# Kernel optimization log

Measured on AMD Instinct MI355X. Metric: run time of the kernel, lower is better.

Reference implementation:

```python
import jax, jax.numpy as jnp
from jax import lax
import numpy as np

T, N, E = 8, 20000, 640000
D_IN, H, K = 2, 64, 3


def setup_inputs() -> dict:
    key = jax.random.key(0)
    ks = jax.random.split(key, 10)
    x = jax.random.normal(ks[0], (T, N, D_IN), dtype=jnp.float32)
    edge_idx = jax.random.randint(ks[1], (T, 2, E), 0, N, dtype=jnp.int64)
    edge_attr = jax.random.uniform(ks[2], (T, E), dtype=jnp.float32)
    Fin = D_IN + H
    s = 0.05
    Wr = jax.random.normal(ks[3], (K, Fin, H), dtype=jnp.float32) * s
    Wu = jax.random.normal(ks[4], (K, Fin, H), dtype=jnp.float32) * s
    Wc = jax.random.normal(ks[5], (K, Fin, H), dtype=jnp.float32) * s
    br = jnp.zeros((H,), dtype=jnp.float32)
    bu = jnp.zeros((H,), dtype=jnp.float32)
    bc = jnp.zeros((H,), dtype=jnp.float32)
    return {"x": x, "edge_idx": edge_idx, "edge_attr": edge_attr,
            "Wr": Wr, "br": br, "Wu": Wu, "bu": bu, "Wc": Wc, "bc": bc}


def reference(x, edge_idx, edge_attr, Wr, br, Wu, bu, Wc, bc):
    n = x.shape[1]
    k_hops = Wr.shape[0]

    def cheb(v, src, dst, wn, W, b):
        # Chebyshev recursion on scaled Laplacian (PyG ChebConv, lambda_max=2)
        def prop(t):
            return jax.ops.segment_sum(wn[:, None] * t[src], dst, num_segments=n)
        Tx0 = v
        out = Tx0 @ W[0]
        Tx1 = prop(Tx0)
        out = out + Tx1 @ W[1]
        for kk in range(2, k_hops):
            Tx2 = 2.0 * prop(Tx1) - Tx0
            out = out + Tx2 @ W[kk]
            Tx0, Tx1 = Tx1, Tx2
        return out + b

    def step(h, inp):
        x_t, ei, w_t = inp
        src, dst = ei[0], ei[1]
        # sym-normalized Laplacian, scaled by 2/lambda_max=1; self-loop weight is 0
        deg = jax.ops.segment_sum(w_t, src, num_segments=n)
        safe = jnp.where(deg > 0, deg, 1.0)
        dinv = jnp.where(deg > 0, lax.rsqrt(safe), 0.0)
        wn = -dinv[src] * w_t * dinv[dst]
        comb = jnp.concatenate([x_t, h], axis=1)
        r = jax.nn.sigmoid(cheb(comb, src, dst, wn, Wr, br))
        u = jax.nn.sigmoid(cheb(comb, src, dst, wn, Wu, bu))
        c = jnp.tanh(cheb(jnp.concatenate([x_t, r * h], axis=1), src, dst, wn, Wc, bc))
        h_new = u * h + (1.0 - u) * c
        return h_new, None

    h0 = jnp.zeros((n, br.shape[0]), dtype=x.dtype)
    h_final, _ = lax.scan(step, h0, (x, edge_idx, edge_attr))
    return h_final
```

## Files before the change

### kernel.cpp

```cpp
#include <hip/hip_runtime.h>

#define NN 20000
#define EE 640000
#define TT 8
#define HF 64
#define AS 232
#define PBLK 5000
#define TILE 2560
#define NBIN 250
#define BWID 80
#define ECAP 3072
#define LCAP 24
#define DCH 32

typedef _Float16 f16;
typedef unsigned int uint;
typedef __attribute__((ext_vector_type(8))) _Float16 half8;
typedef __attribute__((ext_vector_type(4))) float floatx4;

__device__ __forceinline__ float lo16f(uint v) { return (float)__builtin_bit_cast(f16, (unsigned short)(v & 0xffff)); }
__device__ __forceinline__ float hi16f(uint v) { return (float)__builtin_bit_cast(f16, (unsigned short)(v >> 16)); }
__device__ __forceinline__ uint pk16(float a, float b) {
    unsigned short ua = __builtin_bit_cast(unsigned short, (f16)a);
    unsigned short ub = __builtin_bit_cast(unsigned short, (f16)b);
    return (uint)ua | ((uint)ub << 16);
}

__global__ __launch_bounds__(256) void k_prepW(
    const float* __restrict__ Wr, const float* __restrict__ Wu, const float* __restrict__ Wc,
    f16* __restrict__ Wp)
{
    int idx = blockIdx.x * 256 + threadIdx.x;
    if (idx >= 12 * 7 * 64) return;
    int lane = idx & 63;
    int kb = (idx >> 6) % 7;
    int nb = (idx >> 6) / 7;
    int col = nb * 16 + (lane & 15);
    int g = col >> 6, jj = col & 63;
    const float* W = (g == 0) ? Wr : (g == 1 ? Wu : Wc);
    half8 v;
    #pragma unroll
    for (int e = 0; e < 8; e++) {
        int k = kb * 32 + ((lane >> 4) << 3) + e;
        float val = 0.f;
        if (k < 192)      { int hop = k >> 6; int i = 2 + (k & 63); val = W[(hop * 66 + i) * 64 + jj]; }
        else if (k < 198) { int q = k - 192;  int hop = q >> 1;     val = W[(hop * 66 + (q & 1)) * 64 + jj]; }
        v[e] = (f16)val;
    }
    *(half8*)&Wp[(size_t)idx * 8] = v;
}

__global__ __launch_bounds__(256) void k_deg(
    const int* __restrict__ eidx, const float* __restrict__ eatt, int t0,
    float* __restrict__ deg)
{
    __shared__ float dl[NN];
    int tl = blockIdx.x >> 5, chunk = blockIdx.x & (DCH - 1);
    int tid = threadIdx.x;
    for (int n = tid; n < NN; n += 256) dl[n] = 0.f;
    __syncthreads();
    const int*   src = eidx + (size_t)(t0 + tl) * 2 * EE + chunk * (EE / DCH);
    const float* w   = eatt + (size_t)(t0 + tl) * EE + chunk * (EE / DCH);
    for (int e = tid; e < EE / DCH; e += 256) {
        int s = __builtin_nontemporal_load(&src[e]);
        float wv = __builtin_nontemporal_load(&w[e]);
        atomicAdd(&dl[s], wv);
    }
    __syncthreads();
    float* dg = deg + (size_t)tl * NN;
    for (int n = tid; n < NN; n += 256) {
        float v = dl[n];
        if (v != 0.f) atomicAdd(&dg[n], v);
    }
}

__global__ __launch_bounds__(256) void k_dinv_setx(
    float* __restrict__ deg, float* __restrict__ dinv,
    const float* __restrict__ x4, uint* __restrict__ xf4, int* __restrict__ binptr)
{
    int idx = blockIdx.x * 256 + threadIdx.x;
    if (idx < 4 * NBIN) binptr[idx] = 0;
    if (idx >= 4 * NN) return;
    float d = deg[idx];
    deg[idx] = 0.f;
    dinv[idx] = d > 0.f ? 1.f / sqrtf(d) : 0.f;
    int tl = idx / NN, n = idx - tl * NN;
    xf4[idx] = pk16(x4[(size_t)tl * NN * 2 + 2 * n], x4[(size_t)tl * NN * 2 + 2 * n + 1]);
}

__global__ __launch_bounds__(256) void k_bin(
    const int* __restrict__ eidx, const float* __restrict__ eatt, int t0,
    int* __restrict__ binptr, uint2* __restrict__ ebuf)
{
    __shared__ uint2 buf[NBIN][LCAP];
    __shared__ int lcnt[NBIN];
    __shared__ int scan[256];
    __shared__ int gb[NBIN];
    int tid = threadIdx.x;
    if (tid < NBIN) lcnt[tid] = 0;
    __syncthreads();
    int tl = blockIdx.x / 250, tile = blockIdx.x % 250;
    const int*   src = eidx + (size_t)(t0 + tl) * 2 * EE + tile * TILE;
    const int*   dst = src + EE;
    const float* w   = eatt + (size_t)(t0 + tl) * EE + tile * TILE;
    int* bp = binptr + tl * NBIN;
    size_t ebase = (size_t)tl * NBIN * ECAP;
    #pragma unroll
    for (int i = 0; i < TILE / 256; i++) {
        int e = i * 256 + tid;
        int s = __builtin_nontemporal_load(&src[e]);
        int d = __builtin_nontemporal_load(&dst[e]);
        float wv = __builtin_nontemporal_load(&w[e]);
        int bin = d / BWID;
        uint2 ent = make_uint2(((uint)d << 16) | (uint)s, __float_as_uint(wv));
        int p = atomicAdd(&lcnt[bin], 1);
        if (p < LCAP) buf[bin][p] = ent;
        else {
            int gp = atomicAdd(&bp[bin], 1);
            if (gp < ECAP) ebuf[ebase + (size_t)bin * ECAP + gp] = ent;
        }
    }
    __syncthreads();
    int c = (tid < NBIN) ? (lcnt[tid] < LCAP ? lcnt[tid] : LCAP) : 0;
    scan[tid] = c;
    __syncthreads();
    #pragma unroll
    for (int o = 1; o < 256; o <<= 1) {
        int v = (tid >= o) ? scan[tid - o] : 0;
        __syncthreads();
        scan[tid] += v;
        __syncthreads();
    }
    if (c > 0) gb[tid] = atomicAdd(&bp[tid], c);
    __syncthreads();
    int total = scan[255];
    for (int i = tid; i < total; i += 256) {
        int lo = 0, hi = 255;
        #pragma unroll
        for (int it = 0; it < 8; it++) { int mid = (lo + hi) >> 1; if (scan[mid] > i) hi = mid; else lo = mid + 1; }
        int p = i - (lo ? scan[lo - 1] : 0);
        int gp = gb[lo] + p;
        if (gp < ECAP) ebuf[ebase + (size_t)lo * ECAP + gp] = buf[lo][p];
    }
}

__global__ __launch_bounds__(256) void k_csr(
    const uint2* __restrict__ ebuf, const int* __restrict__ binptr,
    const float* __restrict__ dinv,
    uint* __restrict__ entries, int* __restrict__ row_ptr, int* __restrict__ cnt)
{
    __shared__ uint proc[ECAP];
    __shared__ unsigned char lnb[ECAP];
    __shared__ uint staged[ECAP];
    __shared__ int lcnt[BWID], loff[BWID];
    int tl = blockIdx.x / NBIN, b = blockIdx.x % NBIN, tid = threadIdx.x;
    int nume = binptr[tl * NBIN + b]; if (nume > ECAP) nume = ECAP;
    const float* dv = dinv + (size_t)tl * NN;
    size_t base = (size_t)(tl * NBIN + b) * ECAP;
    if (tid < BWID) lcnt[tid] = 0;
    __syncthreads();
    for (int i = tid; i < nume; i += 256) {
        uint2 ent = ebuf[base + i];
        int s = ent.x & 0xffff;
        int d = ent.x >> 16;
        float wv = __uint_as_float(ent.y);
        float wn = -dv[s] * wv * dv[d];
        unsigned short wb = __builtin_bit_cast(unsigned short, (f16)wn);
        proc[i] = ((uint)wb << 16) | (uint)s;
        int ln = d - b * BWID;
        lnb[i] = (unsigned char)ln;
        atomicAdd(&lcnt[ln], 1);
    }
    __syncthreads();
    if (tid == 0) {
        int run = 0;
        for (int i = 0; i < BWID; i++) { loff[i] = run; run += lcnt[i]; }
    }
    __syncthreads();
    if (tid < BWID) {
        int n = tl * NN + b * BWID + tid;
        row_ptr[n] = (int)base + loff[tid];
        cnt[n] = lcnt[tid];
    }
    __syncthreads();
    for (int i = tid; i < nume; i += 256) {
        int p = atomicAdd(&loff[lnb[i]], 1);
        staged[p] = proc[i];
    }
    __syncthreads();
    for (int i = tid; i < nume; i += 256)
        entries[base + i] = staged[i];
}

__global__ __launch_bounds__(256) void k_prop(
    const f16* __restrict__ src_mat, const f16* __restrict__ base,
    f16* __restrict__ dst,
    const int* __restrict__ row_ptr, const int* __restrict__ cnt,
    const uint* __restrict__ entries,
    float alpha, float beta,
    const uint* __restrict__ xsrc, const uint* __restrict__ xbase,
    uint* __restrict__ xdst)
{
    __shared__ uint wnbuf[4][128];
    int ws = threadIdx.x >> 6, lane = threadIdx.x & 63;
    int node = blockIdx.x * 4 + ws;
    int m = cnt[node]; if (m > 128) m = 128;
    int st = row_ptr[node];
    int mp = (m + 15) & ~15;
    for (int idx = lane; idx < mp; idx += 64)
        wnbuf[ws][idx] = (idx < m) ? entries[st + idx] : 0u;
    asm volatile("s_waitcnt lgkmcnt(0)" ::: "memory");

    int j = lane & 31, q = lane >> 5;
    float acc0[8], acc1[8];
    #pragma unroll
    for (int k = 0; k < 8; k++) { acc0[k] = 0.f; acc1[k] = 0.f; }
    for (int e = 0; e < mp; e += 16) {
        uint ee[8], rr[8];
        #pragma unroll
        for (int k = 0; k < 8; k++) ee[k] = wnbuf[ws][e + 2 * k + q];
        #pragma unroll
        for (int k = 0; k < 8; k++) rr[k] = *(const uint*)&src_mat[(size_t)(ee[k] & 0xffff) * HF + 2 * j];
        #pragma unroll
        for (int k = 0; k < 8; k++) {
            float w = hi16f(ee[k]);
            acc0[k] += w * lo16f(rr[k]);
            acc1[k] += w * hi16f(rr[k]);
        }
    }
    float s0 = ((acc0[0] + acc0[1]) + (acc0[2] + acc0[3])) + ((acc0[4] + acc0[5]) + (acc0[6] + acc0[7]));
    float s1 = ((acc1[0] + acc1[1]) + (acc1[2] + acc1[3])) + ((acc1[4] + acc1[5]) + (acc1[6] + acc1[7]));
    s0 += __shfl_xor(s0, 32);
    s1 += __shfl_xor(s1, 32);
    if (q == 0) {
        float r0 = alpha * s0, r1 = alpha * s1;
        if (base) {
            uint bv = *(const uint*)&base[(size_t)node * HF + 2 * j];
            r0 += beta * lo16f(bv);
            r1 += beta * hi16f(bv);
        }
        *(uint*)&dst[(size_t)node * HF + 2 * j] = pk16(r0, r1);
    }

    if (xdst) {
        float xa0 = 0.f, xa1 = 0.f;
        for (int i = lane; i < mp; i += 64) {
            uint ent = wnbuf[ws][i];
            uint xv = xsrc[ent & 0xffff];
            float wn = hi16f(ent);
            xa0 += wn * lo16f(xv);
            xa1 += wn * hi16f(xv);
        }
        #pragma unroll
        for (int o = 32; o >= 1; o >>= 1) {
            xa0 += __shfl_xor(xa0, o);
            xa1 += __shfl_xor(xa1, o);
        }
        if (lane == 0) {
            float r0 = alpha * xa0, r1 = alpha * xa1;
            if (xbase) { uint bv = xbase[node]; r0 += beta * lo16f(bv); r1 += beta * hi16f(bv); }
            xdst[node] = pk16(r0, r1);
        }
    }
}

__device__ __forceinline__ void stage_A(
    f16 (*At)[AS], int n0, int tid, int nthr,
    const f16* h0, const f16* h1, const f16* h2,
    const uint* x0, const uint* x1, const uint* x2)
{
    for (int idx = tid; idx < 64 * 8 * 3; idx += nthr) {
        int a = idx >> 9, r = (idx >> 3) & 63, s = idx & 7;
        const f16* src = (a == 0) ? h0 : (a == 1 ? h1 : h2);
        int gn = n0 + r;
        half8 v = {0, 0, 0, 0, 0, 0, 0, 0};
        if (gn < NN) v = *(const half8*)&src[(size_t)gn * HF + s * 8];
        *(half8*)&At[r][a * 64 + s * 8] = v;
    }
    for (int idx = tid; idx < 64 * 17; idx += nthr) {
        int r = idx / 17, c = idx % 17;
        *(uint*)((char*)&At[r][198] + 4 * c) = 0u;
    }
    for (int idx = tid; idx < 64 * 3; idx += nthr) {
        int r = idx & 63, a = idx >> 6;
        const uint* src = (a == 0) ? x0 : (a == 1 ? x1 : x2);
        int gn = n0 + r;
        uint v = 0;
        if (gn < NN) v = src[gn];
        *(uint*)&At[r][192 + 2 * a] = v;
    }
}

#define MFMA16(a, b, c) __builtin_amdgcn_mfma_f32_16x16x32_f16(a, b, c, 0, 0, 0)

__global__ __launch_bounds__(512) void k_ru(
    const f16* __restrict__ hA, const f16* __restrict__ t1, const f16* __restrict__ t2,
    const uint* __restrict__ xf, const uint* __restrict__ t1x, const uint* __restrict__ t2x,
    const f16* __restrict__ Wp, const float* __restrict__ br, const float* __restrict__ bu,
    f16* __restrict__ u_out, f16* __restrict__ rh_out)
{
    __shared__ __attribute__((aligned(16))) f16 At[64][AS];
    int n0 = blockIdx.x * 64;
    int tid = threadIdx.x;
    stage_A(At, n0, tid, 512, hA, t1, t2, xf, t1x, t2x);
    __syncthreads();

    int wid = tid >> 6, lane = tid & 63;
    int mrow = (wid & 1) * 32;
    int nb0 = (wid >> 1) * 2;
    int arow = mrow + (lane & 15);
    int koff = (lane >> 4) << 3;
    floatx4 z = {0.f, 0.f, 0.f, 0.f};
    floatx4 acc00 = z, acc01 = z, acc10 = z, acc11 = z;
    #pragma unroll
    for (int kb = 0; kb < 7; kb++) {
        half8 a0 = *(const half8*)&At[arow][kb * 32 + koff];
        half8 a1 = *(const half8*)&At[arow + 16][kb * 32 + koff];
        half8 b0 = *(const half8*)&Wp[(size_t)(((nb0    ) * 7 + kb) * 64 + lane) * 8];
        half8 b1 = *(const half8*)&Wp[(size_t)(((nb0 + 1) * 7 + kb) * 64 + lane) * 8];
        acc00 = MFMA16(a0, b0, acc00);
        acc10 = MFMA16(a1, b0, acc10);
        acc01 = MFMA16(a0, b1, acc01);
        acc11 = MFMA16(a1, b1, acc11);
    }
    bool isR = nb0 < 4;
    #pragma unroll
    for (int mi = 0; mi < 2; mi++) {
        #pragma unroll
        for (int ni = 0; ni < 2; ni++) {
            floatx4 a = (mi == 0) ? (ni == 0 ? acc00 : acc01) : (ni == 0 ? acc10 : acc11);
            int jj = ((nb0 + ni) * 16 + (lane & 15)) & 63;
            float bias = isR ? br[jj] : bu[jj];
            int nodeb = n0 + mrow + mi * 16 + ((lane >> 4) << 2);
            #pragma unroll
            for (int e = 0; e < 4; e++) {
                int node = nodeb + e;
                if (node < NN) {
                    float s = 1.f / (1.f + __expf(-(a[e] + bias)));
                    if (isR) {
                        float hv = (float)hA[(size_t)node * HF + jj];
                        rh_out[(size_t)node * HF + jj] = (f16)(s * hv);
                    } else {
                        u_out[(size_t)node * HF + jj] = (f16)s;
                    }
                }
            }
        }
    }
}

__global__ __launch_bounds__(256) void k_c(
    const f16* __restrict__ rh, const f16* __restrict__ t1c, const f16* __restrict__ t2c,
    const uint* __restrict__ xf, const uint* __restrict__ t1x, const uint* __restrict__ t2x,
    const f16* __restrict__ Wp, const float* __restrict__ bc,
    const f16* __restrict__ u_in, const float* __restrict__ h_in,
    float* __restrict__ h_out, f16* __restrict__ hA_out)
{
    __shared__ __attribute__((aligned(16))) f16 At[64][AS];
    int n0 = blockIdx.x * 64;
    int tid = threadIdx.x;
    stage_A(At, n0, tid, 256, rh, t1c, t2c, xf, t1x, t2x);
    __syncthreads();

    int wid = tid >> 6, lane = tid & 63;
    int mrow = (wid & 1) * 32;
    int nb0 = 8 + ((wid >> 1) << 1);
    int arow = mrow + (lane & 15);
    int koff = (lane >> 4) << 3;
    floatx4 z = {0.f, 0.f, 0.f, 0.f};
    floatx4 acc00 = z, acc01 = z, acc10 = z, acc11 = z;
    #pragma unroll
    for (int kb = 0; kb < 7; kb++) {
        half8 a0 = *(const half8*)&At[arow][kb * 32 + koff];
        half8 a1 = *(const half8*)&At[arow + 16][kb * 32 + koff];
        half8 b0 = *(const half8*)&Wp[(size_t)(((nb0    ) * 7 + kb) * 64 + lane) * 8];
        half8 b1 = *(const half8*)&Wp[(size_t)(((nb0 + 1) * 7 + kb) * 64 + lane) * 8];
        acc00 = MFMA16(a0, b0, acc00);
        acc10 = MFMA16(a1, b0, acc10);
        acc01 = MFMA16(a0, b1, acc01);
        acc11 = MFMA16(a1, b1, acc11);
    }
    #pragma unroll
    for (int mi = 0; mi < 2; mi++) {
        #pragma unroll
        for (int ni = 0; ni < 2; ni++) {
            floatx4 a = (mi == 0) ? (ni == 0 ? acc00 : acc01) : (ni == 0 ? acc10 : acc11);
            int jj = (nb0 + ni) * 16 + (lane & 15) - 128;
            float bias = bc[jj];
            int nodeb = n0 + mrow + mi * 16 + ((lane >> 4) << 2);
            #pragma unroll
            for (int e = 0; e < 4; e++) {
                int node = nodeb + e;
                if (node < NN) {
                    float c = tanhf(a[e] + bias);
                    float uu = (float)u_in[(size_t)node * HF + jj];
                    float hp = h_in[(size_t)node * HF + jj];
                    float hn = uu * hp + (1.f - uu) * c;
                    h_out[(size_t)node * HF + jj] = hn;
                    hA_out[(size_t)node * HF + jj] = (f16)hn;
                }
            }
        }
    }
}


extern "C" void kernel_launch(void* const* d_in, const int* in_sizes, int n_in,
                              void* d_out, int out_size, void* d_ws, size_t ws_size,
                              hipStream_t stream)
{
    const float* x    = (const float*)d_in[0];
    const int*   eidx = (const int*)d_in[1];
    const float* eatt = (const float*)d_in[2];
    const float* Wr   = (const float*)d_in[3];
    const float* br   = (const float*)d_in[4];
    const float* Wu   = (const float*)d_in[5];
    const float* bu   = (const float*)d_in[6];
    const float* Wc   = (const float*)d_in[7];
    const float* bc   = (const float*)d_in[8];

    char* ws = (char*)d_ws;
    size_t off = 0;
    auto alloc = [&](size_t bytes) -> void* {
        void* p = ws + off;
        off += (bytes + 255) & ~(size_t)255;
        return p;
    };
    const size_t FB = (size_t)NN * HF * 2;
    float* h_f32  = (float*)alloc((size_t)NN * HF * 4);
    f16*   hA     = (f16*)alloc(FB);
    f16*   t1     = (f16*)alloc(FB);
    f16*   t2     = (f16*)alloc(FB);
    f16*   rh     = (f16*)alloc(FB);
    f16*   u      = (f16*)alloc(FB);
    float* deg    = (float*)alloc((size_t)4 * NN * 4);
    float* dinv   = (float*)alloc((size_t)4 * NN * 4);
    uint*  xf     = (uint*)alloc((size_t)TT * NN * 4);
    uint*  t1x    = (uint*)alloc((size_t)NN * 4);
    uint*  t2x    = (uint*)alloc((size_t)NN * 4);
    int*   binptr = (int*)alloc((size_t)4 * NBIN * 4);
    uint2* ebuf   = (uint2*)alloc((size_t)4 * NBIN * ECAP * 8);
    uint*  entr   = (uint*)alloc((size_t)4 * NBIN * ECAP * 4);
    int*   rowp   = (int*)alloc((size_t)4 * NN * 4);
    int*   cnt    = (int*)alloc((size_t)4 * NN * 4);
    f16*   Wp     = (f16*)alloc((size_t)12 * 7 * 64 * 8 * 2);

    hipMemsetAsync(h_f32, 0, (size_t)NN * HF * 4 + FB, stream);
    hipMemsetAsync(deg, 0, (size_t)4 * NN * 4, stream);
    k_prepW<<<21, 256, 0, stream>>>(Wr, Wu, Wc, Wp);

    const int GB = (NN + 63) / 64;
    const int DB = (4 * NN + 255) / 256;

    for (int half = 0; half < 2; ++half) {
        int t0 = half * 4;
        k_deg      <<<4 * DCH, 256, 0, stream>>>(eidx, eatt, t0, deg);
        k_dinv_setx<<<DB, 256, 0, stream>>>(deg, dinv,
                                            x + (size_t)t0 * NN * 2, xf + (size_t)t0 * NN, binptr);
        k_bin      <<<1000, 256, 0, stream>>>(eidx, eatt, t0, binptr, ebuf);
        k_csr      <<<1000, 256, 0, stream>>>(ebuf, binptr, dinv, entr, rowp, cnt);

        for (int tl = 0; tl < 4; ++tl) {
            int t = t0 + tl;
            const int* rp = rowp + (size_t)tl * NN;
            const int* cp = cnt + (size_t)tl * NN;
            uint* xft = xf + (size_t)t * NN;

            k_prop<<<PBLK, 256, 0, stream>>>(hA, nullptr, t1, rp, cp, entr, 1.f,  0.f, xft, nullptr, t1x);
            k_prop<<<PBLK, 256, 0, stream>>>(t1, hA,      t2, rp, cp, entr, 2.f, -1.f, t1x, xft,     t2x);

            k_ru<<<GB, 512, 0, stream>>>(hA, t1, t2, xft, t1x, t2x, Wp, br, bu, u, rh);

            k_prop<<<PBLK, 256, 0, stream>>>(rh, nullptr, t1, rp, cp, entr, 1.f,  0.f, nullptr, nullptr, nullptr);
            k_prop<<<PBLK, 256, 0, stream>>>(t1, rh,      t2, rp, cp, entr, 2.f, -1.f, nullptr, nullptr, nullptr);

            float* hdst = (t == TT - 1) ? (float*)d_out : h_f32;
            k_c<<<GB, 256, 0, stream>>>(rh, t1, t2, xft, t1x, t2x, Wp, bc, u, h_f32, hdst, hA);
        }
    }
}
```

Before: 811.1 us.

## Reorder candidate Chebyshev conv as transform-then-propagate via Clenshaw, fuse GRU update

```diff
diff --git a/kernel.cpp b/kernel.cpp
--- a/kernel.cpp
+++ b/kernel.cpp
@@ -5,13 +5,15 @@
 #define TT 8
 #define HF 64
 #define AS 232
+#define ACS 104
+#define BSS 194
 #define PBLK 5000
 #define TILE 2560
 #define NBIN 250
 #define BWID 80
 #define ECAP 3072
 #define LCAP 24
-#define DCH 32
+#define DCH 128
 
 typedef _Float16 f16;
 typedef unsigned int uint;
@@ -28,26 +30,48 @@
 
 __global__ __launch_bounds__(256) void k_prepW(
     const float* __restrict__ Wr, const float* __restrict__ Wu, const float* __restrict__ Wc,
-    f16* __restrict__ Wp)
+    f16* __restrict__ Wp, f16* __restrict__ Wcp)
 {
     int idx = blockIdx.x * 256 + threadIdx.x;
-    if (idx >= 12 * 7 * 64) return;
-    int lane = idx & 63;
-    int kb = (idx >> 6) % 7;
-    int nb = (idx >> 6) / 7;
-    int col = nb * 16 + (lane & 15);
-    int g = col >> 6, jj = col & 63;
-    const float* W = (g == 0) ? Wr : (g == 1 ? Wu : Wc);
+    if (idx < 8 * 7 * 64) {
+        int lane = idx & 63;
+        int kb = (idx >> 6) % 7;
+        int nb = (idx >> 6) / 7;
+        int col = nb * 16 + (lane & 15);
+        int g = col >> 6, jj = col & 63;
+        const float* W = (g == 0) ? Wr : Wu;
+        half8 v;
+        #pragma unroll
+        for (int e = 0; e < 8; e++) {
+            int k = kb * 32 + ((lane >> 4) << 3) + e;
+            float val = 0.f;
+            if (k < 192)      { int hop = k >> 6; int i = 2 + (k & 63); val = W[(hop * 66 + i) * 64 + jj]; }
+            else if (k < 198) { int q = k - 192;  int hop = q >> 1;     val = W[(hop * 66 + (q & 1)) * 64 + jj]; }
+            v[e] = (f16)val;
+        }
+        *(half8*)&Wp[(size_t)idx * 8] = v;
+        return;
+    }
+    int idx2 = idx - 8 * 7 * 64;
+    if (idx2 >= 12 * 3 * 64) return;
+    int lane = idx2 & 63;
+    int kb = (idx2 >> 6) % 3;
+    int nbc = (idx2 >> 6) / 3;
+    int col = nbc * 16 + (lane & 15);
+    int mode = col >> 6, j = col & 63;
     half8 v;
     #pragma unroll
     for (int e = 0; e < 8; e++) {
         int k = kb * 32 + ((lane >> 4) << 3) + e;
         float val = 0.f;
-        if (k < 192)      { int hop = k >> 6; int i = 2 + (k & 63); val = W[(hop * 66 + i) * 64 + jj]; }
-        else if (k < 198) { int q = k - 192;  int hop = q >> 1;     val = W[(hop * 66 + (q & 1)) * 64 + jj]; }
+        if (k < 66) {
+            if (mode == 0)      val = Wc[(0 * 66 + k) * 64 + j] - Wc[(2 * 66 + k) * 64 + j];
+            else if (mode == 1) val = Wc[(1 * 66 + k) * 64 + j];
+            else                val = Wc[(2 * 66 + k) * 64 + j];
+        }
         v[e] = (f16)val;
     }
-    *(half8*)&Wp[(size_t)idx * 8] = v;
+    *(half8*)&Wcp[(size_t)idx2 * 8] = v;
 }
 
 __global__ __launch_bounds__(256) void k_deg(
@@ -55,7 +79,7 @@
     float* __restrict__ deg)
 {
     __shared__ float dl[NN];
-    int tl = blockIdx.x >> 5, chunk = blockIdx.x & (DCH - 1);
+    int tl = blockIdx.x >> 7, chunk = blockIdx.x & (DCH - 1);
     int tid = threadIdx.x;
     for (int n = tid; n < NN; n += 256) dl[n] = 0.f;
     __syncthreads();
@@ -192,6 +216,32 @@
         entries[base + i] = staged[i];
 }
 
+__device__ __forceinline__ void gather64(
+    const f16* __restrict__ src_mat, const uint* wnb, int mp, int j, int q,
+    float& s0, float& s1)
+{
+    float acc0[8], acc1[8];
+    #pragma unroll
+    for (int k = 0; k < 8; k++) { acc0[k] = 0.f; acc1[k] = 0.f; }
+    for (int e = 0; e < mp; e += 16) {
+        uint ee[8], rr[8];
+        #pragma unroll
+        for (int k = 0; k < 8; k++) ee[k] = wnb[e + 2 * k + q];
+        #pragma unroll
+        for (int k = 0; k < 8; k++) rr[k] = *(const uint*)&src_mat[(size_t)(ee[k] & 0xffff) * HF + 2 * j];
+        #pragma unroll
+        for (int k = 0; k < 8; k++) {
+            float w = hi16f(ee[k]);
+            acc0[k] += w * lo16f(rr[k]);
+            acc1[k] += w * hi16f(rr[k]);
+        }
+    }
+    s0 = ((acc0[0] + acc0[1]) + (acc0[2] + acc0[3])) + ((acc0[4] + acc0[5]) + (acc0[6] + acc0[7]));
+    s1 = ((acc1[0] + acc1[1]) + (acc1[2] + acc1[3])) + ((acc1[4] + acc1[5]) + (acc1[6] + acc1[7]));
+    s0 += __shfl_xor(s0, 32);
+    s1 += __shfl_xor(s1, 32);
+}
+
 __global__ __launch_bounds__(256) void k_prop(
     const f16* __restrict__ src_mat, const f16* __restrict__ base,
     f16* __restrict__ dst,
@@ -212,26 +262,8 @@
     asm volatile("s_waitcnt lgkmcnt(0)" ::: "memory");
 
     int j = lane & 31, q = lane >> 5;
-    float acc0[8], acc1[8];
-    #pragma unroll
-    for (int k = 0; k < 8; k++) { acc0[k] = 0.f; acc1[k] = 0.f; }
-    for (int e = 0; e < mp; e += 16) {
-        uint ee[8], rr[8];
-        #pragma unroll
-        for (int k = 0; k < 8; k++) ee[k] = wnbuf[ws][e + 2 * k + q];
-        #pragma unroll
-        for (int k = 0; k < 8; k++) rr[k] = *(const uint*)&src_mat[(size_t)(ee[k] & 0xffff) * HF + 2 * j];
-        #pragma unroll
-        for (int k = 0; k < 8; k++) {
-            float w = hi16f(ee[k]);
-            acc0[k] += w * lo16f(rr[k]);
-            acc1[k] += w * hi16f(rr[k]);
-        }
-    }
-    float s0 = ((acc0[0] + acc0[1]) + (acc0[2] + acc0[3])) + ((acc0[4] + acc0[5]) + (acc0[6] + acc0[7]));
-    float s1 = ((acc1[0] + acc1[1]) + (acc1[2] + acc1[3])) + ((acc1[4] + acc1[5]) + (acc1[6] + acc1[7]));
-    s0 += __shfl_xor(s0, 32);
-    s1 += __shfl_xor(s1, 32);
+    float s0, s1;
+    gather64(src_mat, wnbuf[ws], mp, j, q, s0, s1);
     if (q == 0) {
         float r0 = alpha * s0, r1 = alpha * s1;
         if (base) {
@@ -264,45 +296,84 @@
     }
 }
 
-__device__ __forceinline__ void stage_A(
-    f16 (*At)[AS], int n0, int tid, int nthr,
-    const f16* h0, const f16* h1, const f16* h2,
-    const uint* x0, const uint* x1, const uint* x2)
-{
-    for (int idx = tid; idx < 64 * 8 * 3; idx += nthr) {
+__global__ __launch_bounds__(256) void k_prop_fin(
+    const f16* __restrict__ S, const f16* __restrict__ B0,
+    const f16* __restrict__ u, const float* __restrict__ h_in,
+    float* __restrict__ h_out, f16* __restrict__ hA_out,
+    const int* __restrict__ row_ptr, const int* __restrict__ cnt,
+    const uint* __restrict__ entries)
+{
+    __shared__ uint wnbuf[4][128];
+    int ws = threadIdx.x >> 6, lane = threadIdx.x & 63;
+    int node = blockIdx.x * 4 + ws;
+    int m = cnt[node]; if (m > 128) m = 128;
+    int st = row_ptr[node];
+    int mp = (m + 15) & ~15;
+    for (int idx = lane; idx < mp; idx += 64)
+        wnbuf[ws][idx] = (idx < m) ? entries[st + idx] : 0u;
+    asm volatile("s_waitcnt lgkmcnt(0)" ::: "memory");
+
+    int j = lane & 31, q = lane >> 5;
+    float s0, s1;
+    gather64(S, wnbuf[ws], mp, j, q, s0, s1);
+    if (q == 0) {
+        uint b0v = *(const uint*)&B0[(size_t)node * HF + 2 * j];
+        float c0 = tanhf(s0 + lo16f(b0v));
+        float c1 = tanhf(s1 + hi16f(b0v));
+        uint uv = *(const uint*)&u[(size_t)node * HF + 2 * j];
+        float u0 = lo16f(uv), u1 = hi16f(uv);
+        float2 hv = *(const float2*)&h_in[(size_t)node * HF + 2 * j];
+        float hn0 = u0 * hv.x + (1.f - u0) * c0;
+        float hn1 = u1 * hv.y + (1.f - u1) * c1;
+        *(float2*)&h_out[(size_t)node * HF + 2 * j] = make_float2(hn0, hn1);
+        *(uint*)&hA_out[(size_t)node * HF + 2 * j] = pk16(hn0, hn1);
+    }
+}
+
+#define MFMA16(a, b, c) __builtin_amdgcn_mfma_f32_16x16x32_f16(a, b, c, 0, 0, 0)
+
+__global__ __launch_bounds__(512) void k_ru(
+    const f16* __restrict__ hA, const f16* __restrict__ t1, const f16* __restrict__ t2,
+    const uint* __restrict__ xf, const uint* __restrict__ t1x, const uint* __restrict__ t2x,
+    const f16* __restrict__ Wp, const f16* __restrict__ Wcp,
+    const float* __restrict__ br, const float* __restrict__ bu, const float* __restrict__ bc,
+    f16* __restrict__ u_out,
+    f16* __restrict__ B0, f16* __restrict__ B1, f16* __restrict__ B2)
+{
+    __shared__ __attribute__((aligned(16))) f16 At[64][AS];
+    __shared__ __attribute__((aligned(16))) f16 Ac[64][ACS];
+    __shared__ f16 Ub[64][68];
+    int n0 = blockIdx.x * 64;
+    int tid = threadIdx.x;
+
+    for (int idx = tid; idx < 64 * 8 * 3; idx += 512) {
         int a = idx >> 9, r = (idx >> 3) & 63, s = idx & 7;
-        const f16* src = (a == 0) ? h0 : (a == 1 ? h1 : h2);
+        const f16* src = (a == 0) ? hA : (a == 1 ? t1 : t2);
         int gn = n0 + r;
         half8 v = {0, 0, 0, 0, 0, 0, 0, 0};
         if (gn < NN) v = *(const half8*)&src[(size_t)gn * HF + s * 8];
         *(half8*)&At[r][a * 64 + s * 8] = v;
     }
-    for (int idx = tid; idx < 64 * 17; idx += nthr) {
+    for (int idx = tid; idx < 64 * 17; idx += 512) {
         int r = idx / 17, c = idx % 17;
         *(uint*)((char*)&At[r][198] + 4 * c) = 0u;
     }
-    for (int idx = tid; idx < 64 * 3; idx += nthr) {
+    for (int idx = tid; idx < 64 * 3; idx += 512) {
         int r = idx & 63, a = idx >> 6;
-        const uint* src = (a == 0) ? x0 : (a == 1 ? x1 : x2);
+        const uint* src = (a == 0) ? xf : (a == 1 ? t1x : t2x);
         int gn = n0 + r;
         uint v = 0;
         if (gn < NN) v = src[gn];
         *(uint*)&At[r][192 + 2 * a] = v;
     }
-}
-
-#define MFMA16(a, b, c) __builtin_amdgcn_mfma_f32_16x16x32_f16(a, b, c, 0, 0, 0)
-
-__global__ __launch_bounds__(512) void k_ru(
-    const f16* __restrict__ hA, const f16* __restrict__ t1, const f16* __restrict__ t2,
-    const uint* __restrict__ xf, const uint* __restrict__ t1x, const uint* __restrict__ t2x,
-    const f16* __restrict__ Wp, const float* __restrict__ br, const float* __restrict__ bu,
-    f16* __restrict__ u_out, f16* __restrict__ rh_out)
-{
-    __shared__ __attribute__((aligned(16))) f16 At[64][AS];
-    int n0 = blockIdx.x * 64;
-    int tid = threadIdx.x;
-    stage_A(At, n0, tid, 512, hA, t1, t2, xf, t1x, t2x);
+    for (int idx = tid; idx < 64; idx += 512) {
+        int gn = n0 + idx;
+        *(uint*)&Ac[idx][0] = (gn < NN) ? xf[gn] : 0u;
+    }
+    for (int idx = tid; idx < 64 * 15; idx += 512) {
+        int r = idx / 15, c = idx % 15;
+        *(uint*)((char*)&Ac[r][66] + 4 * c) = 0u;
+    }
     __syncthreads();
 
     int wid = tid >> 6, lane = tid & 63;
@@ -311,95 +382,79 @@
     int arow = mrow + (lane & 15);
     int koff = (lane >> 4) << 3;
     floatx4 z = {0.f, 0.f, 0.f, 0.f};
-    floatx4 acc00 = z, acc01 = z, acc10 = z, acc11 = z;
-    #pragma unroll
-    for (int kb = 0; kb < 7; kb++) {
-        half8 a0 = *(const half8*)&At[arow][kb * 32 + koff];
-        half8 a1 = *(const half8*)&At[arow + 16][kb * 32 + koff];
-        half8 b0 = *(const half8*)&Wp[(size_t)(((nb0    ) * 7 + kb) * 64 + lane) * 8];
-        half8 b1 = *(const half8*)&Wp[(size_t)(((nb0 + 1) * 7 + kb) * 64 + lane) * 8];
-        acc00 = MFMA16(a0, b0, acc00);
-        acc10 = MFMA16(a1, b0, acc10);
-        acc01 = MFMA16(a0, b1, acc01);
-        acc11 = MFMA16(a1, b1, acc11);
-    }
-    bool isR = nb0 < 4;
-    #pragma unroll
-    for (int mi = 0; mi < 2; mi++) {
-        #pragma unroll
-        for (int ni = 0; ni < 2; ni++) {
-            floatx4 a = (mi == 0) ? (ni == 0 ? acc00 : acc01) : (ni == 0 ? acc10 : acc11);
-            int jj = ((nb0 + ni) * 16 + (lane & 15)) & 63;
-            float bias = isR ? br[jj] : bu[jj];
-            int nodeb = n0 + mrow + mi * 16 + ((lane >> 4) << 2);
+    {
+        floatx4 acc00 = z, acc01 = z, acc10 = z, acc11 = z;
+        #pragma unroll
+        for (int kb = 0; kb < 7; kb++) {
+            half8 a0 = *(const half8*)&At[arow][kb * 32 + koff];
+            half8 a1 = *(const half8*)&At[arow + 16][kb * 32 + koff];
+            half8 b0 = *(const half8*)&Wp[(size_t)(((nb0    ) * 7 + kb) * 64 + lane) * 8];
+            half8 b1 = *(const half8*)&Wp[(size_t)(((nb0 + 1) * 7 + kb) * 64 + lane) * 8];
+            acc00 = MFMA16(a0, b0, acc00);
+            acc10 = MFMA16(a1, b0, acc10);
+            acc01 = MFMA16(a0, b1, acc01);
+            acc11 = MFMA16(a1, b1, acc11);
+        }
+        bool isR = nb0 < 4;
+        #pragma unroll
+        for (int mi = 0; mi < 2; mi++) {
             #pragma unroll
-            for (int e = 0; e < 4; e++) {
-                int node = nodeb + e;
-                if (node < NN) {
+            for (int ni = 0; ni < 2; ni++) {
+                floatx4 a = (mi == 0) ? (ni == 0 ? acc00 : acc01) : (ni == 0 ? acc10 : acc11);
+                int jj = ((nb0 + ni) * 16 + (lane & 15)) & 63;
+                float bias = isR ? br[jj] : bu[jj];
+                int rbase = mrow + mi * 16 + ((lane >> 4) << 2);
+                #pragma unroll
+                for (int e = 0; e < 4; e++) {
+                    int rloc = rbase + e;
                     float s = 1.f / (1.f + __expf(-(a[e] + bias)));
                     if (isR) {
-                        float hv = (float)hA[(size_t)node * HF + jj];
-                        rh_out[(size_t)node * HF + jj] = (f16)(s * hv);
+                        float hv = (float)At[rloc][jj];
+                        Ac[rloc][2 + jj] = (f16)(s * hv);
                     } else {
-                        u_out[(size_t)node * HF + jj] = (f16)s;
+                        Ub[rloc][jj] = (f16)s;
                     }
                 }
             }
         }
     }
-}
-
-__global__ __launch_bounds__(256) void k_c(
-    const f16* __restrict__ rh, const f16* __restrict__ t1c, const f16* __restrict__ t2c,
-    const uint* __restrict__ xf, const uint* __restrict__ t1x, const uint* __restrict__ t2x,
-    const f16* __restrict__ Wp, const float* __restrict__ bc,
-    const f16* __restrict__ u_in, const float* __restrict__ h_in,
-    float* __restrict__ h_out, f16* __restrict__ hA_out)
-{
-    __shared__ __attribute__((aligned(16))) f16 At[64][AS];
-    int n0 = blockIdx.x * 64;
-    int tid = threadIdx.x;
-    stage_A(At, n0, tid, 256, rh, t1c, t2c, xf, t1x, t2x);
-    __syncthreads();
-
-    int wid = tid >> 6, lane = tid & 63;
-    int mrow = (wid & 1) * 32;
-    int nb0 = 8 + ((wid >> 1) << 1);
-    int arow = mrow + (lane & 15);
-    int koff = (lane >> 4) << 3;
-    floatx4 z = {0.f, 0.f, 0.f, 0.f};
-    floatx4 acc00 = z, acc01 = z, acc10 = z, acc11 = z;
+    __syncthreads();
+
+    for (int idx = tid; idx < 64 * 32; idx += 512) {
+        int n = idx >> 5, c = idx & 31;
+        int gn = n0 + n;
+        if (gn < NN) *(uint*)&u_out[(size_t)gn * HF + 2 * c] = *(uint*)&Ub[n][2 * c];
+    }
+    f16* Bs = &At[0][0];
     #pragma unroll
-    for (int kb = 0; kb < 7; kb++) {
-        half8 a0 = *(const half8*)&At[arow][kb * 32 + koff];
-        half8 a1 = *(const half8*)&At[arow + 16][kb * 32 + koff];
-        half8 b0 = *(const half8*)&Wp[(size_t)(((nb0    ) * 7 + kb) * 64 + lane) * 8];
-        half8 b1 = *(const half8*)&Wp[(size_t)(((nb0 + 1) * 7 + kb) * 64 + lane) * 8];
-        acc00 = MFMA16(a0, b0, acc00);
-        acc10 = MFMA16(a1, b0, acc10);
-        acc01 = MFMA16(a0, b1, acc01);
-        acc11 = MFMA16(a1, b1, acc11);
-    }
-    #pragma unroll
-    for (int mi = 0; mi < 2; mi++) {
-        #pragma unroll
-        for (int ni = 0; ni < 2; ni++) {
-            floatx4 a = (mi == 0) ? (ni == 0 ? acc00 : acc01) : (ni == 0 ? acc10 : acc11);
-            int jj = (nb0 + ni) * 16 + (lane & 15) - 128;
-            float bias = bc[jj];
-            int nodeb = n0 + mrow + mi * 16 + ((lane >> 4) << 2);
-            #pragma unroll
-            for (int e = 0; e < 4; e++) {
-                int node = nodeb + e;
-                if (node < NN) {
-                    float c = tanhf(a[e] + bias);
-                    float uu = (float)u_in[(size_t)node * HF + jj];
-                    float hp = h_in[(size_t)node * HF + jj];
-                    float hn = uu * hp + (1.f - uu) * c;
-                    h_out[(size_t)node * HF + jj] = hn;
-                    hA_out[(size_t)node * HF + jj] = (f16)hn;
-                }
-            }
+    for (int i = 0; i < 6; i++) {
+        int t = wid * 6 + i;
+        int nbc = t >> 2, mq = t & 3;
+        int ar = mq * 16 + (lane & 15);
+        floatx4 acc;
+        float binit = (nbc < 4) ? bc[nbc * 16 + (lane & 15)] : 0.f;
+        acc[0] = binit; acc[1] = binit; acc[2] = binit; acc[3] = binit;
+        #pragma unroll
+        for (int kb = 0; kb < 3; kb++) {
+            half8 a = *(const half8*)&Ac[ar][kb * 32 + koff];
+            half8 b = *(const half8*)&Wcp[(size_t)(((nbc * 3 + kb) * 64) + lane) * 8];
+            acc = MFMA16(a, b, acc);
+        }
+        int rbase = mq * 16 + ((lane >> 4) << 2);
+        int col = nbc * 16 + (lane & 15);
+        #pragma unroll
+        for (int e = 0; e < 4; e++)
+            Bs[(size_t)(rbase + e) * BSS + col] = (f16)acc[e];
+    }
+    __syncthreads();
+
+    for (int idx = tid; idx < 64 * 96; idx += 512) {
+        int n = idx / 96, c = idx % 96;
+        int gn = n0 + n;
+        if (gn < NN) {
+            int col = 2 * c;
+            f16* Bdst = (col < 64) ? B0 : (col < 128 ? B1 : B2);
+            *(uint*)&Bdst[(size_t)gn * HF + (col & 63)] = *(uint*)&Bs[(size_t)n * BSS + col];
         }
     }
 }
@@ -431,8 +486,10 @@
     f16*   hA     = (f16*)alloc(FB);
     f16*   t1     = (f16*)alloc(FB);
     f16*   t2     = (f16*)alloc(FB);
-    f16*   rh     = (f16*)alloc(FB);
     f16*   u      = (f16*)alloc(FB);
+    f16*   B0     = (f16*)alloc(FB);
+    f16*   B1     = (f16*)alloc(FB);
+    f16*   B2     = (f16*)alloc(FB);
     float* deg    = (float*)alloc((size_t)4 * NN * 4);
     float* dinv   = (float*)alloc((size_t)4 * NN * 4);
     uint*  xf     = (uint*)alloc((size_t)TT * NN * 4);
@@ -443,11 +500,12 @@
     uint*  entr   = (uint*)alloc((size_t)4 * NBIN * ECAP * 4);
     int*   rowp   = (int*)alloc((size_t)4 * NN * 4);
     int*   cnt    = (int*)alloc((size_t)4 * NN * 4);
-    f16*   Wp     = (f16*)alloc((size_t)12 * 7 * 64 * 8 * 2);
+    f16*   Wp     = (f16*)alloc((size_t)8 * 7 * 64 * 8 * 2);
+    f16*   Wcp    = (f16*)alloc((size_t)12 * 3 * 64 * 8 * 2);
 
     hipMemsetAsync(h_f32, 0, (size_t)NN * HF * 4 + FB, stream);
     hipMemsetAsync(deg, 0, (size_t)4 * NN * 4, stream);
-    k_prepW<<<21, 256, 0, stream>>>(Wr, Wu, Wc, Wp);
+    k_prepW<<<30, 256, 0, stream>>>(Wr, Wu, Wc, Wp, Wcp);
 
     const int GB = (NN + 63) / 64;
     const int DB = (4 * NN + 255) / 256;
@@ -469,13 +527,13 @@
             k_prop<<<PBLK, 256, 0, stream>>>(hA, nullptr, t1, rp, cp, entr, 1.f,  0.f, xft, nullptr, t1x);
             k_prop<<<PBLK, 256, 0, stream>>>(t1, hA,      t2, rp, cp, entr, 2.f, -1.f, t1x, xft,     t2x);
 
-            k_ru<<<GB, 512, 0, stream>>>(hA, t1, t2, xft, t1x, t2x, Wp, br, bu, u, rh);
-
-            k_prop<<<PBLK, 256, 0, stream>>>(rh, nullptr, t1, rp, cp, entr, 1.f,  0.f, nullptr, nullptr, nullptr);
-            k_prop<<<PBLK, 256, 0, stream>>>(t1, rh,      t2, rp, cp, entr, 2.f, -1.f, nullptr, nullptr, nullptr);
+            k_ru<<<GB, 512, 0, stream>>>(hA, t1, t2, xft, t1x, t2x, Wp, Wcp,
+                                         br, bu, bc, u, B0, B1, B2);
+
+            k_prop<<<PBLK, 256, 0, stream>>>(B2, B1, t2, rp, cp, entr, 2.f, 1.f, nullptr, nullptr, nullptr);
 
             float* hdst = (t == TT - 1) ? (float*)d_out : h_f32;
-            k_c<<<GB, 256, 0, stream>>>(rh, t1, t2, xft, t1x, t2x, Wp, bc, u, h_f32, hdst, hA);
-        }
-    }
-}
+            k_prop_fin<<<PBLK, 256, 0, stream>>>(t2, B0, u, h_f32, hdst, hA, rp, cp, entr);
+        }
+    }
+}
```

Result: faster. 760.8 us (-6.2%).
